# Kernel optimization log

Hardware: AMD Instinct MI355X
Metric: run time of the kernel (lower is better)

Reference implementation:

```python
import jax, jax.numpy as jnp
import numpy as np

N_CLOUDS = 16
N_PTS = 2048
K = 5            # spline kernel_size per dim
KC = K ** 3      # 125 kernel weights
BITS = np.array([[i & 1, (i >> 1) & 1, (i >> 2) & 1] for i in range(8)])  # degree-1 B-spline corners


def _radius_edges_np(pos, batch, r, max_nb=32):
    # brute-force radius graph, up to max_nb nearest neighbors within r, no self loops
    srcs, tgts = [], []
    for c in np.unique(batch):
        ids = np.where(batch == c)[0]
        P = pos[ids]
        D = np.linalg.norm(P[:, None, :] - P[None, :, :], axis=-1).astype(np.float32)
        np.fill_diagonal(D, np.inf)
        D[D > r] = np.inf
        order = np.argsort(D, axis=1)[:, :max_nb]
        valid = np.isfinite(np.take_along_axis(D, order, axis=1))
        tgt_loc = np.broadcast_to(np.arange(len(ids))[:, None], order.shape)
        srcs.append(ids[order[valid]])
        tgts.append(ids[tgt_loc[valid]])
    return np.concatenate(srcs).astype(np.int32), np.concatenate(tgts).astype(np.int32)


def _fps_np(pos, batch, ratio):
    out = []
    for c in np.unique(batch):
        ids = np.where(batch == c)[0]
        P = pos[ids]
        m = int(round(ratio * len(ids)))
        sel = [0]
        d = np.linalg.norm(P - P[0], axis=1)
        for _ in range(m - 1):
            i = int(d.argmax())
            sel.append(i)
            d = np.minimum(d, np.linalg.norm(P - P[i], axis=1))
        out.append(ids[np.array(sel)])
    return np.concatenate(out).astype(np.int32)


def setup_inputs() -> dict:
    rng = np.random.default_rng(0)
    pos = rng.random((N_CLOUDS * N_PTS, 3)).astype(np.float32)
    batch = np.repeat(np.arange(N_CLOUDS), N_PTS).astype(np.int32)

    src1, tgt1 = _radius_edges_np(pos, batch, 0.2)
    idx1 = _fps_np(pos, batch, 0.5)
    pos2, batch2 = pos[idx1], batch[idx1]
    src2, tgt2 = _radius_edges_np(pos2, batch2, 0.4)
    idx2 = _fps_np(pos2, batch2, 0.25)
    pos3, batch3 = pos2[idx2], batch2[idx2]
    src3, tgt3 = _radius_edges_np(pos3, batch3, 1.0)

    def p(shape, scale=0.1):
        return (rng.standard_normal(shape) * scale).astype(np.float32)

    inp = {
        'pos': jnp.asarray(pos), 'batch': jnp.asarray(batch),
        'src1': jnp.asarray(src1), 'tgt1': jnp.asarray(tgt1),
        'src2': jnp.asarray(src2), 'tgt2': jnp.asarray(tgt2),
        'src3': jnp.asarray(src3), 'tgt3': jnp.asarray(tgt3),
        'idx1': jnp.asarray(idx1), 'idx2': jnp.asarray(idx2),
        'W1': jnp.asarray(p((KC, 1, 64))),  'R1': jnp.asarray(p((1, 64))),   'b1': jnp.zeros((64,), jnp.float32),
        'W2': jnp.asarray(p((KC, 64, 64))), 'R2': jnp.asarray(p((64, 64))),  'b2': jnp.zeros((64,), jnp.float32),
        'W3': jnp.asarray(p((KC, 64, 128))),'R3': jnp.asarray(p((64, 128))), 'b3': jnp.zeros((128,), jnp.float32),
        'lw1': jnp.asarray(p((128, 256))), 'lb1': jnp.zeros((256,), jnp.float32),
        'lw2': jnp.asarray(p((256, 256))), 'lb2': jnp.zeros((256,), jnp.float32),
        'lw3': jnp.asarray(p((256, 10))),  'lb3': jnp.zeros((10,), jnp.float32),
    }
    return inp


def _pseudo(pos, src, tgt, r):
    return jnp.clip((pos[tgt] - pos[src]) / (2.0 * r) + 0.5, 0.0, 1.0)


def _spline_conv(x, pseudo, src, tgt, n, W, R, b):
    # SplineConv: degree-1 open B-spline basis, mean aggregation, root weight + bias
    Cin = x.shape[1]
    v = pseudo * (K - 1)                  # [E,3]
    bot = jnp.floor(v)
    frac = v - bot                        # [E,3]
    boti = bot.astype(jnp.int32)
    xj = x[src]                           # [E,Cin]
    A = jnp.zeros((n * KC, Cin), x.dtype)
    for s in range(8):                    # 8 nonzero basis products per edge
        bits = BITS[s]
        w = jnp.where(bits == 1, frac, 1.0 - frac).prod(-1)     # [E]
        idx = jnp.clip(boti + bits, 0, K - 1)                   # [E,3]
        wi = idx[:, 0] + K * idx[:, 1] + K * K * idx[:, 2]      # [E]
        A = A.at[tgt * KC + wi].add(w[:, None] * xj)
    A = A.reshape(n, KC, Cin)             # per-node per-kernel accumulated features
    msg = jnp.einsum('nkc,kco->no', A, W)
    deg = jax.ops.segment_sum(jnp.ones(tgt.shape[0], x.dtype), tgt, num_segments=n)
    msg = msg / jnp.maximum(deg, 1.0)[:, None]
    return msg + x @ R + b


def reference(pos, batch, src1, tgt1, src2, tgt2, src3, tgt3, idx1, idx2,
              W1, R1, b1, W2, R2, b2, W3, R3, b3,
              lw1, lb1, lw2, lb2, lw3, lb3):
    n1 = pos.shape[0]
    x = jnp.ones((n1, 1), pos.dtype)
    x = jax.nn.elu(_spline_conv(x, _pseudo(pos, src1, tgt1, 0.2), src1, tgt1, n1, W1, R1, b1))
    x, pos2 = x[idx1], pos[idx1]
    n2 = pos2.shape[0]
    x = jax.nn.elu(_spline_conv(x, _pseudo(pos2, src2, tgt2, 0.4), src2, tgt2, n2, W2, R2, b2))
    x, pos3 = x[idx2], pos2[idx2]
    n3 = pos3.shape[0]
    x = jax.nn.elu(_spline_conv(x, _pseudo(pos3, src3, tgt3, 1.0), src3, tgt3, n3, W3, R3, b3))
    batch3 = batch[idx1][idx2]
    num = jax.ops.segment_sum(x, batch3, num_segments=N_CLOUDS)
    cnt = jax.ops.segment_sum(jnp.ones(n3, x.dtype), batch3, num_segments=N_CLOUDS)
    g = num / jnp.maximum(cnt, 1.0)[:, None]          # global_mean_pool [16,128]
    h = jax.nn.elu(g @ lw1 + lb1)
    h = jax.nn.elu(h @ lw2 + lb2)
    # dropout is identity in eval mode
    logits = h @ lw3 + lb3
    return jax.nn.log_softmax(logits, axis=-1)
```

## Files before the change

kernel.cpp:

```cpp
#include <hip/hip_runtime.h>
#include <hip/hip_bf16.h>
#include <math.h>

#define KDIM 5
#define KC 125
#define KPAD 8192
#define EPB 32
#define NSPLIT 4
#define LDA 72
#define SSTR 40
#define XSTR 40
#define H1STR 40

typedef short bf16x8 __attribute__((ext_vector_type(8)));
typedef float f32x4 __attribute__((ext_vector_type(4)));

__device__ __forceinline__ float elu_f(float x) { return x > 0.f ? x : (expf(x) - 1.f); }

__device__ __forceinline__ void fadd_atomic(float* p, float v) {
    unsafeAtomicAdd(p, v);
}

__device__ __forceinline__ unsigned short f2bf(float x) {
    union { float f; unsigned u; } v; v.f = x;
    unsigned r = (v.u + 0x7FFFu + ((v.u >> 16) & 1u)) >> 16;
    return (unsigned short)r;
}
__device__ __forceinline__ unsigned pack2(float lo, float hi) {
    __hip_bfloat162 h = __float22bfloat162_rn(make_float2(lo, hi));
    unsigned r; __builtin_memcpy(&r, &h, 4); return r;
}

__global__ void rowptr_kernel(const int* __restrict__ tgt, int E, int n, int* __restrict__ rowptr)
{
    int e = blockIdx.x * blockDim.x + threadIdx.x;
    if (e > E) return;
    if (e < E) {
        int t = tgt[e];
        int p = (e == 0) ? -1 : tgt[e - 1];
        for (int v = p + 1; v <= t; v++) rowptr[v] = e;
    } else {
        int p = tgt[E - 1];
        for (int v = p + 1; v <= n; v++) rowptr[v] = E;
    }
}

__global__ void slots_kernel(const float* __restrict__ posL, const int* __restrict__ src,
                             const int* __restrict__ tgt, int E, float rinv2, int sinkrow,
                             unsigned* __restrict__ slots)
{
    int e = blockIdx.x * blockDim.x + threadIdx.x;
    if (e >= E) return;
    int s = src[e], t = tgt[e];
    float p0 = fminf(fmaxf((posL[t*3+0] - posL[s*3+0]) * rinv2 + 0.5f, 0.f), 1.f);
    float p1 = fminf(fmaxf((posL[t*3+1] - posL[s*3+1]) * rinv2 + 0.5f, 0.f), 1.f);
    float p2 = fminf(fmaxf((posL[t*3+2] - posL[s*3+2]) * rinv2 + 0.5f, 0.f), 1.f);
    float v0 = p0 * (KDIM - 1), v1 = p1 * (KDIM - 1), v2 = p2 * (KDIM - 1);
    int b0 = (int)floorf(v0), b1 = (int)floorf(v1), b2 = (int)floorf(v2);
    float f0 = v0 - (float)b0, f1 = v1 - (float)b1, f2 = v2 - (float)b2;
    unsigned out[8];
    #pragma unroll
    for (int sb = 0; sb < 8; sb++) {
        int i0 = sb & 1, i1 = (sb >> 1) & 1, i2 = (sb >> 2) & 1;
        float w = (i0 ? f0 : 1.f - f0) * (i1 ? f1 : 1.f - f1) * (i2 ? f2 : 1.f - f2);
        int k0 = min(b0 + i0, KDIM - 1), k1 = min(b1 + i1, KDIM - 1), k2 = min(b2 + i2, KDIM - 1);
        int wi = k0 + KDIM * k1 + KDIM * KDIM * k2;
        if (w == 0.f) wi = sinkrow;
        out[sb] = (__float_as_uint(w) & ~127u) | (unsigned)wi;
    }
    uint4* dst = (uint4*)&slots[(size_t)e * 8];
    dst[0] = make_uint4(out[0], out[1], out[2], out[3]);
    dst[1] = make_uint4(out[4], out[5], out[6], out[7]);
}

__global__ __launch_bounds__(256) void histo1_kernel(const unsigned* __restrict__ slots,
                                                     const int* __restrict__ rowptr,
                                                     unsigned short* __restrict__ Aout)
{
    __shared__ __attribute__((aligned(16))) unsigned short S[4][128 * H1STR];
    int wave = threadIdx.x >> 6, lane = threadIdx.x & 63;
    int node = blockIdx.x * 4 + wave;
    int rs = rowptr[node], re = rowptr[node + 1];
    int deg = re - rs;
    unsigned short* Sw = S[wave];

    for (int i = lane; i < 128 * H1STR / 8; i += 64)
        ((uint4*)Sw)[i] = make_uint4(0, 0, 0, 0);

    int wbase = lane * 4;
    if (wbase < deg * 8) {
        uint4 sw = *(const uint4*)&slots[(size_t)rs * 8 + wbase];
        unsigned wd[4] = {sw.x, sw.y, sw.z, sw.w};
        #pragma unroll
        for (int j = 0; j < 4; j++) {
            int e = (wbase + j) >> 3;
            int wi = wd[j] & 127u;
            Sw[wi * H1STR + e] = f2bf(__uint_as_float(wd[j] & ~127u));
        }
    }
    __syncthreads();

    const short one = 0x3F80;
    bf16x8 bones = {one, one, one, one, one, one, one, one};
    int fr = lane & 15, fq = (lane >> 4) * 8;
    f32x4 acc[8];
    #pragma unroll
    for (int tl = 0; tl < 8; tl++) {
        bf16x8 af = *(const bf16x8*)&Sw[(tl * 16 + fr) * H1STR + fq];
        acc[tl] = __builtin_amdgcn_mfma_f32_16x16x32_bf16(
            af, bones, (f32x4){0.f, 0.f, 0.f, 0.f}, 0, 0, 0);
    }

    float invdeg = 1.f / fmaxf((float)deg, 1.f);
    if ((lane & 15) == 0) {
        int rbase = (lane >> 4) * 4;
        #pragma unroll
        for (int tl = 0; tl < 8; tl++)
            #pragma unroll
            for (int r = 0; r < 4; r++) {
                int row = tl * 16 + rbase + r;
                float v = (row < KC) ? acc[tl][r] * invdeg : (row == KC ? 1.f : 0.f);
                Sw[row] = f2bf(v);
            }
    }
    __syncthreads();
    unsigned lo = Sw[2 * lane], hi = Sw[2 * lane + 1];
    ((unsigned*)(Aout + (size_t)node * 128))[lane] = lo | (hi << 16);
}

__global__ __launch_bounds__(256) void buildA_kernel(
    const unsigned* __restrict__ slots, const int* __restrict__ src,
    const int* __restrict__ rowptr, const unsigned short* __restrict__ xbf,
    int nodeBase, unsigned short* __restrict__ Aout)
{
    __shared__ __attribute__((aligned(16))) unsigned short S[128 * SSTR];
    __shared__ __attribute__((aligned(16))) unsigned short XT[64 * XSTR];
    __shared__ int Es[EPB];
    int node = nodeBase + blockIdx.x;
    int t = threadIdx.x;
    int rs = rowptr[node], re = rowptr[node + 1];
    int ne = re - rs;
    int wave = t >> 6, lane = t & 63;
    int fr = lane & 15, fq = (lane >> 4) * 8;

    for (int i = t; i < 128 * SSTR / 2; i += 256) ((unsigned*)S)[i] = 0;
    for (int i = t; i < 64 * XSTR / 2; i += 256) ((unsigned*)XT)[i] = 0;
    if (t < ne) Es[t] = src[rs + t];
    __syncthreads();
    if (t < ne * 8) {
        int e = t >> 3;
        unsigned word = slots[(size_t)rs * 8 + t];
        int wi = word & 127u;
        S[wi * SSTR + e] = f2bf(__uint_as_float(word & ~127u));
    }
    for (int i = t; i < ne * 64; i += 256) {
        int c = i & 63, el = i >> 6;
        XT[c * XSTR + el] = xbf[(size_t)Es[el] * 64 + c];
    }
    __syncthreads();

    f32x4 acc[2][4];
    #pragma unroll
    for (int i = 0; i < 2; i++)
        #pragma unroll
        for (int j = 0; j < 4; j++) acc[i][j] = (f32x4){0.f, 0.f, 0.f, 0.f};
    #pragma unroll
    for (int i = 0; i < 2; i++) {
        bf16x8 af = *(const bf16x8*)&S[((2 * wave + i) * 16 + fr) * SSTR + fq];
        #pragma unroll
        for (int j = 0; j < 4; j++) {
            bf16x8 bg = *(const bf16x8*)&XT[(j * 16 + fr) * XSTR + fq];
            acc[i][j] = __builtin_amdgcn_mfma_f32_16x16x32_bf16(af, bg, acc[i][j], 0, 0, 0);
        }
    }

    float invdeg = 1.f / fmaxf((float)ne, 1.f);
    unsigned short* out = Aout + (size_t)blockIdx.x * KPAD;
    int quad = lane >> 4;
    #pragma unroll
    for (int i = 0; i < 2; i++) {
        int wibase = (2 * wave + i) * 16 + quad * 4;
        #pragma unroll
        for (int r = 0; r < 4; r++) {
            int wi = wibase + r;
            if (wi < KC) {
                #pragma unroll
                for (int j = 0; j < 4; j++)
                    out[wi * 64 + j * 16 + fr] = f2bf(acc[i][j][r] * invdeg);
            }
        }
    }
    if (t < 64) out[8000 + t] = xbf[(size_t)node * 64 + t];
    if (t < 128) out[8064 + t] = 0;
}

__global__ void concatWT_kernel(const float* __restrict__ W, const float* __restrict__ R,
                                int COUT, int kpad, int krows, int cin,
                                unsigned short* __restrict__ WfT)
{
    int i = blockIdx.x * blockDim.x + threadIdx.x;
    if (i >= COUT * kpad) return;
    int n = i / kpad, k = i - n * kpad;
    float v = 0.f;
    if (k < krows) v = W[(size_t)k * COUT + n];
    else if (k < krows + cin) v = R[(size_t)(k - krows) * COUT + n];
    WfT[i] = f2bf(v);
}

__global__ __launch_bounds__(256) void gemm_kernel(const unsigned short* __restrict__ A,
                                                   const unsigned short* __restrict__ BT,
                                                   int Mrows, int COUT, int Ksz, int lda,
                                                   float* __restrict__ P)
{
    __shared__ __attribute__((aligned(16))) unsigned short As[2 * 64 * LDA];
    __shared__ __attribute__((aligned(16))) unsigned short Bs[2 * 64 * LDA];
    int t = threadIdx.x;
    int mblk = blockIdx.x * 64, nblk = blockIdx.y * 64;
    int kBase = blockIdx.z * Ksz;

    int lr = t >> 2;
    int lc = (t & 3) * 16;

    const unsigned short* Ap = A + (size_t)(mblk + lr) * lda + kBase + lc;
    const unsigned short* Bp = BT + (size_t)(nblk + lr) * lda + kBase + lc;

    uint4 a0 = *(const uint4*)Ap;  uint4 a1 = *(const uint4*)(Ap + 8);
    uint4 b0 = *(const uint4*)Bp;  uint4 b1 = *(const uint4*)(Bp + 8);

    int wave = t >> 6, lane = t & 63;
    int mw = (wave & 1) * 32, nw = (wave >> 1) * 32;
    int fr = lane & 15;
    int fq = (lane >> 4) * 8;

    f32x4 acc[2][2];
    #pragma unroll
    for (int i = 0; i < 2; i++)
        #pragma unroll
        for (int j = 0; j < 2; j++) acc[i][j] = (f32x4){0.f, 0.f, 0.f, 0.f};

    *(uint4*)&As[lr * LDA + lc]     = a0;
    *(uint4*)&As[lr * LDA + lc + 8] = a1;
    *(uint4*)&Bs[lr * LDA + lc]     = b0;
    *(uint4*)&Bs[lr * LDA + lc + 8] = b1;
    __syncthreads();

    int ktiles = Ksz / 64;
    for (int kt = 0; kt < ktiles; kt++) {
        int cur = (kt & 1) * 64 * LDA;
        if (kt + 1 < ktiles) {
            Ap += 64; Bp += 64;
            a0 = *(const uint4*)Ap; a1 = *(const uint4*)(Ap + 8);
            b0 = *(const uint4*)Bp; b1 = *(const uint4*)(Bp + 8);
        }
        #pragma unroll
        for (int ks = 0; ks < 2; ks++) {
            bf16x8 af0 = *(const bf16x8*)&As[cur + (mw + fr) * LDA + ks * 32 + fq];
            bf16x8 af1 = *(const bf16x8*)&As[cur + (mw + 16 + fr) * LDA + ks * 32 + fq];
            bf16x8 bg0 = *(const bf16x8*)&Bs[cur + (nw + fr) * LDA + ks * 32 + fq];
            bf16x8 bg1 = *(const bf16x8*)&Bs[cur + (nw + 16 + fr) * LDA + ks * 32 + fq];
            acc[0][0] = __builtin_amdgcn_mfma_f32_16x16x32_bf16(af0, bg0, acc[0][0], 0, 0, 0);
            acc[0][1] = __builtin_amdgcn_mfma_f32_16x16x32_bf16(af0, bg1, acc[0][1], 0, 0, 0);
            acc[1][0] = __builtin_amdgcn_mfma_f32_16x16x32_bf16(af1, bg0, acc[1][0], 0, 0, 0);
            acc[1][1] = __builtin_amdgcn_mfma_f32_16x16x32_bf16(af1, bg1, acc[1][1], 0, 0, 0);
        }
        if (kt + 1 < ktiles) {
            int nxt = ((kt + 1) & 1) * 64 * LDA;
            *(uint4*)&As[nxt + lr * LDA + lc]     = a0;
            *(uint4*)&As[nxt + lr * LDA + lc + 8] = a1;
            *(uint4*)&Bs[nxt + lr * LDA + lc]     = b0;
            *(uint4*)&Bs[nxt + lr * LDA + lc + 8] = b1;
        }
        __syncthreads();
    }
    float* Pz = P + (size_t)blockIdx.z * Mrows * COUT;
    int crow = (lane >> 4) * 4, ccol = lane & 15;
    #pragma unroll
    for (int i = 0; i < 2; i++)
        #pragma unroll
        for (int j = 0; j < 2; j++) {
            int m0 = mblk + mw + i * 16 + crow;
            int n0 = nblk + nw + j * 16 + ccol;
            #pragma unroll
            for (int r = 0; r < 4; r++)
                Pz[(size_t)(m0 + r) * COUT + n0] = acc[i][j][r];
        }
}

__global__ void combine_kernel(const float* __restrict__ P, const float* __restrict__ b,
                               int Mrows, int COUT, int NS, float* __restrict__ xout)
{
    int i = blockIdx.x * blockDim.x + threadIdx.x;
    int total = Mrows * COUT;
    if (i >= total) return;
    float s = 0.f;
    for (int z = 0; z < NS; z++) s += P[(size_t)z * total + i];
    int o = i % COUT;
    xout[i] = elu_f(s + b[o]);
}

__global__ void xgather_kernel(const float* __restrict__ x_src, const int* __restrict__ idx,
                               int n, unsigned short* __restrict__ x_dst)
{
    int tid = blockIdx.x * blockDim.x + threadIdx.x;
    if (tid >= n * 64) return;
    int i = tid >> 6, c = tid & 63;
    x_dst[tid] = f2bf(x_src[(size_t)idx[i] * 64 + c]);
}

__global__ void posgather_kernel(const float* __restrict__ pos_src, const int* __restrict__ idx,
                                 int n, float* __restrict__ pos_dst)
{
    int tid = blockIdx.x * blockDim.x + threadIdx.x;
    if (tid >= n * 3) return;
    int i = tid / 3, d = tid - i * 3;
    pos_dst[tid] = pos_src[idx[i] * 3 + d];
}

__global__ void zero_kernel(float* __restrict__ p, int n)
{
    int i = blockIdx.x * blockDim.x + threadIdx.x;
    if (i < n) p[i] = 0.f;
}

__global__ void cid_kernel(const int* __restrict__ batch, const int* __restrict__ idx1,
                           const int* __restrict__ idx2, int n3,
                           int* __restrict__ cid, float* __restrict__ cnt)
{
    __shared__ int h[16];
    int t = threadIdx.x;
    int i = blockIdx.x * 256 + t;
    if (t < 16) h[t] = 0;
    __syncthreads();
    if (i < n3) {
        int cl = batch[idx1[idx2[i]]];
        cid[i] = cl;
        atomicAdd(&h[cl], 1);
    }
    __syncthreads();
    if (t < 16 && h[t] > 0) fadd_atomic(&cnt[t], (float)h[t]);
}

__global__ void pool2_kernel(const float* __restrict__ x3, const int* __restrict__ cid,
                             int n3, float* __restrict__ gnum)
{
    int t = threadIdx.x;
    int c = t & 127, h = t >> 7;
    int base = blockIdx.x * 64;
    int nn = min(64, n3 - base);
    float sum = 0.f; int cur = -1;
    for (int j = h; j < nn; j += 2) {
        int i = base + j;
        int cl = cid[i];
        if (cl != cur) {
            if (cur >= 0) fadd_atomic(&gnum[cur * 128 + c], sum);
            cur = cl; sum = 0.f;
        }
        sum += x3[(size_t)i * 128 + c];
    }
    if (cur >= 0) fadd_atomic(&gnum[cur * 128 + c], sum);
}

__global__ void mlp_kernel(const float* __restrict__ gnum, const float* __restrict__ cnt,
                           const float* __restrict__ lw1, const float* __restrict__ lb1,
                           const float* __restrict__ lw2, const float* __restrict__ lb2,
                           const float* __restrict__ lw3, const float* __restrict__ lb3,
                           float* __restrict__ out)
{
    __shared__ float gv[128], h1[256], h2[256], lg[10];
    __shared__ float lse_s;
    int cl = blockIdx.x, t = threadIdx.x;
    if (t < 128) gv[t] = gnum[cl * 128 + t] / fmaxf(cnt[cl], 1.f);
    __syncthreads();
    float a = lb1[t];
    for (int c = 0; c < 128; c++) a += gv[c] * lw1[c * 256 + t];
    h1[t] = elu_f(a);
    __syncthreads();
    a = lb2[t];
    for (int c = 0; c < 256; c++) a += h1[c] * lw2[c * 256 + t];
    h2[t] = elu_f(a);
    __syncthreads();
    if (t < 10) {
        a = lb3[t];
        for (int c = 0; c < 256; c++) a += h2[c] * lw3[c * 10 + t];
        lg[t] = a;
    }
    __syncthreads();
    if (t == 0) {
        float m = -1e30f;
        for (int i = 0; i < 10; i++) m = fmaxf(m, lg[i]);
        float s = 0.f;
        for (int i = 0; i < 10; i++) s += expf(lg[i] - m);
        lse_s = m + logf(s);
    }
    __syncthreads();
    if (t < 10) out[cl * 10 + t] = lg[t] - lse_s;
}

static void run_level(const unsigned* slots, const int* src, const int* rowptr,
                      const unsigned short* xbf, const unsigned short* WfT, const float* bvec,
                      int n, int COUT, unsigned short* Abuf, int AbufRows, float* P,
                      float* xout, hipStream_t stream)
{
    int Ksz = KPAD / NSPLIT;
    for (int cs = 0; cs < n; cs += AbufRows) {
        int cr = min(AbufRows, n - cs);
        buildA_kernel<<<cr, 256, 0, stream>>>(slots, src, rowptr, xbf, cs, Abuf);
        dim3 grid(cr / 64, COUT / 64, NSPLIT);
        gemm_kernel<<<grid, 256, 0, stream>>>(Abuf, WfT, cr, COUT, Ksz, KPAD, P);
        combine_kernel<<<(cr * COUT + 255) / 256, 256, 0, stream>>>(P, bvec, cr, COUT, NSPLIT,
                                                                    xout + (size_t)cs * COUT);
    }
}

extern "C" void kernel_launch(void* const* d_in, const int* in_sizes, int n_in,
                              void* d_out, int out_size, void* d_ws, size_t ws_size,
                              hipStream_t stream)
{
    const float* pos   = (const float*)d_in[0];
    const int*   batch = (const int*)d_in[1];
    const int*   src1  = (const int*)d_in[2];
    const int*   tgt1  = (const int*)d_in[3];
    const int*   src2  = (const int*)d_in[4];
    const int*   tgt2  = (const int*)d_in[5];
    const int*   src3  = (const int*)d_in[6];
    const int*   tgt3  = (const int*)d_in[7];
    const int*   idx1  = (const int*)d_in[8];
    const int*   idx2  = (const int*)d_in[9];
    const float* W1 = (const float*)d_in[10];
    const float* R1 = (const float*)d_in[11];
    const float* b1 = (const float*)d_in[12];
    const float* W2 = (const float*)d_in[13];
    const float* R2 = (const float*)d_in[14];
    const float* b2 = (const float*)d_in[15];
    const float* W3 = (const float*)d_in[16];
    const float* R3 = (const float*)d_in[17];
    const float* b3 = (const float*)d_in[18];
    const float* lw1 = (const float*)d_in[19];
    const float* lb1 = (const float*)d_in[20];
    const float* lw2 = (const float*)d_in[21];
    const float* lb2 = (const float*)d_in[22];
    const float* lw3 = (const float*)d_in[23];
    const float* lb3 = (const float*)d_in[24];

    int n1 = in_sizes[0] / 3;
    int E1 = in_sizes[2];
    int E2 = in_sizes[4];
    int E3 = in_sizes[6];
    int n2 = in_sizes[8];
    int n3 = in_sizes[9];

    float* ws = (float*)d_ws;
    float* x1   = ws;
    float* x2o  = x1   + (size_t)n1 * 64;
    float* x3o  = x2o  + (size_t)n2 * 64;
    float* pos2 = x3o  + (size_t)n3 * 128;
    float* pos3 = pos2 + (size_t)n2 * 3;
    float* gnum = pos3 + (size_t)n3 * 3;
    float* cnt  = gnum + 16 * 128;
    int*   cid  = (int*)(cnt + 16);
    unsigned short* x2in = (unsigned short*)(cid + ((n3 + 4) & ~3));
    unsigned short* x3in = x2in + (size_t)n2 * 64;
    unsigned short* WfT1 = x3in + (size_t)n3 * 64;
    unsigned short* WfT2 = WfT1 + (size_t)64 * 128;
    unsigned short* WfT3 = WfT2 + (size_t)64 * KPAD;
    int*   rp1  = (int*)(WfT3 + (size_t)128 * KPAD);
    int*   rp2  = rp1 + ((n1 + 4) & ~3);
    int*   rp3  = rp2 + ((n2 + 4) & ~3);
    unsigned* slots1 = (unsigned*)(rp3 + ((n3 + 4) & ~3));
    unsigned* slots2 = slots1 + (size_t)E1 * 8;
    unsigned* slots3 = slots2 + (size_t)E2 * 8;
    unsigned short* A1buf = (unsigned short*)(slots3 + (size_t)E3 * 8);
    float*  P    = (float*)(A1buf + (size_t)n1 * 128);
    unsigned short* Abuf = (unsigned short*)(P + (size_t)8 * 1024 * 1024);

    size_t usedBytes = (size_t)((char*)Abuf - (char*)ws);
    size_t availBytes = ws_size > usedBytes ? ws_size - usedBytes : 0;
    int maxRows = (int)(availBytes / ((size_t)KPAD * 2));
    maxRows &= ~63;
    if (maxRows < 64) maxRows = 64;
    int rowsP2 = ((8 * 1024 * 1024) / (NSPLIT * 64)) & ~63;
    int rowsP3 = ((8 * 1024 * 1024) / (NSPLIT * 128)) & ~63;
    int rows2 = min(min(maxRows, rowsP2), n2);
    int rows3 = min(min(maxRows, rowsP3), n3);

    float* out = (float*)d_out;

    rowptr_kernel<<<(E1 + 256) / 256, 256, 0, stream>>>(tgt1, E1, n1, rp1);
    rowptr_kernel<<<(E2 + 256) / 256, 256, 0, stream>>>(tgt2, E2, n2, rp2);
    rowptr_kernel<<<(E3 + 256) / 256, 256, 0, stream>>>(tgt3, E3, n3, rp3);
    posgather_kernel<<<(n2 * 3 + 255) / 256, 256, 0, stream>>>(pos, idx1, n2, pos2);
    posgather_kernel<<<(n3 * 3 + 255) / 256, 256, 0, stream>>>(pos2, idx2, n3, pos3);
    slots_kernel<<<(E1 + 255) / 256, 256, 0, stream>>>(pos,  src1, tgt1, E1, 2.5f,  126, slots1);
    slots_kernel<<<(E2 + 255) / 256, 256, 0, stream>>>(pos2, src2, tgt2, E2, 1.25f, 125, slots2);
    slots_kernel<<<(E3 + 255) / 256, 256, 0, stream>>>(pos3, src3, tgt3, E3, 0.5f,  125, slots3);
    concatWT_kernel<<<(64 * 128 + 255) / 256, 256, 0, stream>>>(W1, R1, 64, 128, KC, 1, WfT1);
    concatWT_kernel<<<(64 * KPAD + 255) / 256, 256, 0, stream>>>(W2, R2, 64, KPAD, KC * 64, 64, WfT2);
    concatWT_kernel<<<(128 * KPAD + 255) / 256, 256, 0, stream>>>(W3, R3, 128, KPAD, KC * 64, 64, WfT3);

    zero_kernel<<<(16 * 128 + 16 + 255) / 256, 256, 0, stream>>>(gnum, 16 * 128 + 16);
    cid_kernel<<<(n3 + 255) / 256, 256, 0, stream>>>(batch, idx1, idx2, n3, cid, cnt);

    histo1_kernel<<<n1 / 4, 256, 0, stream>>>(slots1, rp1, A1buf);
    {
        dim3 g1(n1 / 64, 1, 1);
        gemm_kernel<<<g1, 256, 0, stream>>>(A1buf, WfT1, n1, 64, 128, 128, P);
        combine_kernel<<<(n1 * 64 + 255) / 256, 256, 0, stream>>>(P, b1, n1, 64, 1, x1);
    }
    xgather_kernel<<<(n2 * 64 + 255) / 256, 256, 0, stream>>>(x1, idx1, n2, x2in);

    run_level(slots2, src2, rp2, x2in, WfT2, b2, n2, 64, Abuf, rows2, P, x2o, stream);
    xgather_kernel<<<(n3 * 64 + 255) / 256, 256, 0, stream>>>(x2o, idx2, n3, x3in);

    run_level(slots3, src3, rp3, x3in, WfT3, b3, n3, 128, Abuf, rows3, P, x3o, stream);

    pool2_kernel<<<(n3 + 63) / 64, 256, 0, stream>>>(x3o, cid, n3, gnum);
    mlp_kernel<<<16, 256, 0, stream>>>(gnum, cnt, lw1, lb1, lw2, lb2, lw3, lb3, out);
}
```

Measured before the change: 416.5 us.

## Merge setup kernels into multi-batch launches and double GEMM split-K

Several small preprocessing kernels (rowptr, slots, position gather, weight transpose) are merged into single launches that use blockIdx.y to pick the level. This cuts launch count and per-launch overhead. A composed idx1[idx2] index is computed once and reused for pos3 and cluster ids. NSPLIT goes from 4 to 8, which raises the split-K parallelism of the level GEMMs but adds partial-sum traffic and may shrink the rows per chunk.

```diff
diff --git a/kernel.cpp b/kernel.cpp
--- a/kernel.cpp
+++ b/kernel.cpp
@@ -6,7 +6,7 @@
 #define KC 125
 #define KPAD 8192
 #define EPB 32
-#define NSPLIT 4
+#define NSPLIT 8
 #define LDA 72
 #define SSTR 40
 #define XSTR 40
@@ -31,8 +31,14 @@
     unsigned r; __builtin_memcpy(&r, &h, 4); return r;
 }
 
-__global__ void rowptr_kernel(const int* __restrict__ tgt, int E, int n, int* __restrict__ rowptr)
-{
+__global__ void rowptr3_kernel(const int* __restrict__ t1, int E1, int n1, int* __restrict__ r1,
+                               const int* __restrict__ t2, int E2, int n2, int* __restrict__ r2,
+                               const int* __restrict__ t3, int E3, int n3, int* __restrict__ r3)
+{
+    const int* tgt; int E, n; int* rowptr;
+    if (blockIdx.y == 0)      { tgt = t1; E = E1; n = n1; rowptr = r1; }
+    else if (blockIdx.y == 1) { tgt = t2; E = E2; n = n2; rowptr = r2; }
+    else                      { tgt = t3; E = E3; n = n3; rowptr = r3; }
     int e = blockIdx.x * blockDim.x + threadIdx.x;
     if (e > E) return;
     if (e < E) {
@@ -45,11 +51,11 @@
     }
 }
 
-__global__ void slots_kernel(const float* __restrict__ posL, const int* __restrict__ src,
-                             const int* __restrict__ tgt, int E, float rinv2, int sinkrow,
-                             unsigned* __restrict__ slots)
-{
-    int e = blockIdx.x * blockDim.x + threadIdx.x;
+__device__ __forceinline__ void slots_body(const float* __restrict__ posL,
+                                           const int* __restrict__ src,
+                                           const int* __restrict__ tgt, int E, float rinv2,
+                                           int sinkrow, unsigned* __restrict__ slots, int e)
+{
     if (e >= E) return;
     int s = src[e], t = tgt[e];
     float p0 = fminf(fmaxf((posL[t*3+0] - posL[s*3+0]) * rinv2 + 0.5f, 0.f), 1.f);
@@ -73,6 +79,22 @@
     dst[1] = make_uint4(out[4], out[5], out[6], out[7]);
 }
 
+__global__ void slots3_kernel(const float* __restrict__ posA, const int* __restrict__ sA,
+                              const int* __restrict__ tA, int EA, float rA, int kA,
+                              unsigned* __restrict__ oA,
+                              const float* __restrict__ posB, const int* __restrict__ sB,
+                              const int* __restrict__ tB, int EB, float rB, int kB,
+                              unsigned* __restrict__ oB,
+                              const float* __restrict__ posC, const int* __restrict__ sC,
+                              const int* __restrict__ tC, int EC, float rC, int kC,
+                              unsigned* __restrict__ oC)
+{
+    int e = blockIdx.x * blockDim.x + threadIdx.x;
+    if (blockIdx.y == 0)      slots_body(posA, sA, tA, EA, rA, kA, oA, e);
+    else if (blockIdx.y == 1) slots_body(posB, sB, tB, EB, rB, kB, oB, e);
+    else                      slots_body(posC, sC, tC, EC, rC, kC, oC, e);
+}
+
 __global__ __launch_bounds__(256) void histo1_kernel(const unsigned* __restrict__ slots,
                                                      const int* __restrict__ rowptr,
                                                      unsigned short* __restrict__ Aout)
@@ -207,6 +229,23 @@
     WfT[i] = f2bf(v);
 }
 
+__global__ void concatWT23_kernel(const float* __restrict__ W2, const float* __restrict__ R2,
+                                  unsigned short* __restrict__ WfT2,
+                                  const float* __restrict__ W3, const float* __restrict__ R3,
+                                  unsigned short* __restrict__ WfT3)
+{
+    const float* W; const float* R; unsigned short* WfT; int COUT;
+    if (blockIdx.y == 0) { W = W2; R = R2; WfT = WfT2; COUT = 64; }
+    else                 { W = W3; R = R3; WfT = WfT3; COUT = 128; }
+    int i = blockIdx.x * blockDim.x + threadIdx.x;
+    if (i >= COUT * KPAD) return;
+    int n = i >> 13, k = i & (KPAD - 1);
+    float v = 0.f;
+    if (k < KC * 64) v = W[(size_t)k * COUT + n];
+    else if (k < KC * 64 + 64) v = R[(size_t)(k - KC * 64) * COUT + n];
+    WfT[i] = f2bf(v);
+}
+
 __global__ __launch_bounds__(256) void gemm_kernel(const unsigned short* __restrict__ A,
                                                    const unsigned short* __restrict__ BT,
                                                    int Mrows, int COUT, int Ksz, int lda,
@@ -307,13 +346,28 @@
     x_dst[tid] = f2bf(x_src[(size_t)idx[i] * 64 + c]);
 }
 
-__global__ void posgather_kernel(const float* __restrict__ pos_src, const int* __restrict__ idx,
-                                 int n, float* __restrict__ pos_dst)
+__global__ void posgather2_kernel(const float* __restrict__ pos, const int* __restrict__ idx1,
+                                  int n2, float* __restrict__ pos2,
+                                  const int* __restrict__ idx12, int n3,
+                                  float* __restrict__ pos3)
 {
     int tid = blockIdx.x * blockDim.x + threadIdx.x;
-    if (tid >= n * 3) return;
-    int i = tid / 3, d = tid - i * 3;
-    pos_dst[tid] = pos_src[idx[i] * 3 + d];
+    if (blockIdx.y == 0) {
+        if (tid >= n2 * 3) return;
+        int i = tid / 3, d = tid - i * 3;
+        pos2[tid] = pos[idx1[i] * 3 + d];
+    } else {
+        if (tid >= n3 * 3) return;
+        int i = tid / 3, d = tid - i * 3;
+        pos3[tid] = pos[idx12[i] * 3 + d];
+    }
+}
+
+__global__ void composeidx_kernel(const int* __restrict__ idx1, const int* __restrict__ idx2,
+                                  int n3, int* __restrict__ idx12)
+{
+    int i = blockIdx.x * blockDim.x + threadIdx.x;
+    if (i < n3) idx12[i] = idx1[idx2[i]];
 }
 
 __global__ void zero_kernel(float* __restrict__ p, int n)
@@ -322,9 +376,8 @@
     if (i < n) p[i] = 0.f;
 }
 
-__global__ void cid_kernel(const int* __restrict__ batch, const int* __restrict__ idx1,
-                           const int* __restrict__ idx2, int n3,
-                           int* __restrict__ cid, float* __restrict__ cnt)
+__global__ void cid_kernel(const int* __restrict__ batch, const int* __restrict__ idx12,
+                           int n3, int* __restrict__ cid, float* __restrict__ cnt)
 {
     __shared__ int h[16];
     int t = threadIdx.x;
@@ -332,7 +385,7 @@
     if (t < 16) h[t] = 0;
     __syncthreads();
     if (i < n3) {
-        int cl = batch[idx1[idx2[i]]];
+        int cl = batch[idx12[i]];
         cid[i] = cl;
         atomicAdd(&h[cl], 1);
     }
@@ -458,7 +511,8 @@
     float* gnum = pos3 + (size_t)n3 * 3;
     float* cnt  = gnum + 16 * 128;
     int*   cid  = (int*)(cnt + 16);
-    unsigned short* x2in = (unsigned short*)(cid + ((n3 + 4) & ~3));
+    int*   idx12 = cid + ((n3 + 4) & ~3);
+    unsigned short* x2in = (unsigned short*)(idx12 + ((n3 + 4) & ~3));
     unsigned short* x3in = x2in + (size_t)n2 * 64;
     unsigned short* WfT1 = x3in + (size_t)n3 * 64;
     unsigned short* WfT2 = WfT1 + (size_t)64 * 128;
@@ -485,20 +539,31 @@
 
     float* out = (float*)d_out;
 
-    rowptr_kernel<<<(E1 + 256) / 256, 256, 0, stream>>>(tgt1, E1, n1, rp1);
-    rowptr_kernel<<<(E2 + 256) / 256, 256, 0, stream>>>(tgt2, E2, n2, rp2);
-    rowptr_kernel<<<(E3 + 256) / 256, 256, 0, stream>>>(tgt3, E3, n3, rp3);
-    posgather_kernel<<<(n2 * 3 + 255) / 256, 256, 0, stream>>>(pos, idx1, n2, pos2);
-    posgather_kernel<<<(n3 * 3 + 255) / 256, 256, 0, stream>>>(pos2, idx2, n3, pos3);
-    slots_kernel<<<(E1 + 255) / 256, 256, 0, stream>>>(pos,  src1, tgt1, E1, 2.5f,  126, slots1);
-    slots_kernel<<<(E2 + 255) / 256, 256, 0, stream>>>(pos2, src2, tgt2, E2, 1.25f, 125, slots2);
-    slots_kernel<<<(E3 + 255) / 256, 256, 0, stream>>>(pos3, src3, tgt3, E3, 0.5f,  125, slots3);
+    {
+        dim3 g((E1 + 256) / 256, 3);
+        rowptr3_kernel<<<g, 256, 0, stream>>>(tgt1, E1, n1, rp1,
+                                              tgt2, E2, n2, rp2,
+                                              tgt3, E3, n3, rp3);
+    }
+    composeidx_kernel<<<(n3 + 255) / 256, 256, 0, stream>>>(idx1, idx2, n3, idx12);
+    {
+        dim3 g((n2 * 3 + 255) / 256, 2);
+        posgather2_kernel<<<g, 256, 0, stream>>>(pos, idx1, n2, pos2, idx12, n3, pos3);
+    }
+    {
+        dim3 g((E1 + 255) / 256, 3);
+        slots3_kernel<<<g, 256, 0, stream>>>(pos,  src1, tgt1, E1, 2.5f,  126, slots1,
+                                             pos2, src2, tgt2, E2, 1.25f, 125, slots2,
+                                             pos3, src3, tgt3, E3, 0.5f,  125, slots3);
+    }
     concatWT_kernel<<<(64 * 128 + 255) / 256, 256, 0, stream>>>(W1, R1, 64, 128, KC, 1, WfT1);
-    concatWT_kernel<<<(64 * KPAD + 255) / 256, 256, 0, stream>>>(W2, R2, 64, KPAD, KC * 64, 64, WfT2);
-    concatWT_kernel<<<(128 * KPAD + 255) / 256, 256, 0, stream>>>(W3, R3, 128, KPAD, KC * 64, 64, WfT3);
+    {
+        dim3 g((128 * KPAD + 255) / 256, 2);
+        concatWT23_kernel<<<g, 256, 0, stream>>>(W2, R2, WfT2, W3, R3, WfT3);
+    }
 
     zero_kernel<<<(16 * 128 + 16 + 255) / 256, 256, 0, stream>>>(gnum, 16 * 128 + 16);
-    cid_kernel<<<(n3 + 255) / 256, 256, 0, stream>>>(batch, idx1, idx2, n3, cid, cnt);
+    cid_kernel<<<(n3 + 255) / 256, 256, 0, stream>>>(batch, idx12, n3, cid, cnt);
 
     histo1_kernel<<<n1 / 4, 256, 0, stream>>>(slots1, rp1, A1buf);
     {
```

Result: slower. 451.9 us (+8.5%).
